# Optimization experiments

Hardware: AMD Instinct MI355X
Metric: run time of the kernel (lower is better)

Reference implementation:

```python
import jax, jax.numpy as jnp
import numpy as np

KMEANS_ITERS = 10  # fixed Lloyd iterations (original kmeans_pytorch iterates to tolerance)


def _assign(X, cent):
    # squared euclidean distances [N, K] (argmin identical to euclidean)
    d = (jnp.sum(X * X, axis=1, keepdims=True)
         - 2.0 * X @ cent.T
         + jnp.sum(cent * cent, axis=1)[None, :])
    return jnp.argmin(d, axis=1)


def _kmeans(X, K, iters, key):
    N, _ = X.shape
    init_idx = jax.random.choice(key, N, (K,), replace=False)
    cent0 = X[init_idx]

    def step(cent, _):
        idx = _assign(X, cent)
        sums = jax.ops.segment_sum(X, idx, num_segments=K)
        cnt = jax.ops.segment_sum(jnp.ones((N,), X.dtype), idx, num_segments=K)
        new = jnp.where(cnt[:, None] > 0,
                        sums / jnp.maximum(cnt, 1.0)[:, None],
                        cent)
        return new, None

    cent, _ = jax.lax.scan(step, cent0, None, length=iters)
    return _assign(X, cent)


def setup_inputs() -> dict:
    key = jax.random.key(0)
    B, L, D, H = 2, 4096, 256, 8
    k1, k2 = jax.random.split(key)
    qk = jax.random.normal(k1, (B, L, D), dtype=jnp.float32)
    # nn.init.orthogonal_ on (B, D, D): flatten to (B, D*D), make rows orthonormal.
    G = jax.random.normal(k2, (D * D, B), dtype=jnp.float32)
    Q, _ = jnp.linalg.qr(G)                # (D*D, B) orthonormal columns
    W_R = Q.T.reshape(B, D, D)             # rows orthonormal across batch
    return {"qk": qk, "W_R": W_R, "n_heads": H}


def reference(qk, W_R, n_heads):
    qk = jax.lax.stop_gradient(qk)          # qk.detach()
    B, L, D = qk.shape
    R = jnp.einsum('bld,bde->ble', qk, W_R).reshape(B * L, D)
    K = int(L ** 0.5)
    idx = _kmeans(R, K, KMEANS_ITERS, jax.random.key(42))
    cid = idx.reshape(B, L)
    # same-cluster mask [B, 1, L, L] broadcast to heads
    same = (cid[:, None, :, None] == cid[:, None, None, :])
    mask = jnp.broadcast_to(same, (B, n_heads, L, L)).astype(jnp.float32)
    return 10000.0 * mask - 10000.0
```

## Files before the change

kernel.cpp:

```cpp
#include <hip/hip_runtime.h>
#include <stdint.h>
#include <stddef.h>
#include <vector>
#include <algorithm>
#include <utility>

#define NPTS 8192
#define DIM  256
#define KC   64
#define LSEQ 4096
#define NB   2
#define KM_ITERS 10
#define NCHUNK 64
#define NBLK 128
#define NCENT 64
#define XPITCH 260
#define PPITCH 257

#define JAX_THREEFRY_PARTITIONABLE 1

__device__ float g_R[NPTS * DIM];
__device__ float g_xsq[NPTS];
__device__ float g_centT[DIM * KC];
__device__ float g_csq[KC];
__device__ int   g_idx[NPTS];

__device__ unsigned g_arrive[NBLK * 16];
__device__ unsigned g_release_arr[NBLK * 16];

__device__ __forceinline__ void grid_barrier(int c, unsigned target) {
  __syncthreads();
  const int t = threadIdx.x;
  if (t == 0) {
    __hip_atomic_store(&g_arrive[c * 16], target, __ATOMIC_RELEASE,
                       __HIP_MEMORY_SCOPE_AGENT);
  }
  if (c == 0) {
    if (t < NBLK) {
      while (__hip_atomic_load(&g_arrive[t * 16], __ATOMIC_RELAXED,
                               __HIP_MEMORY_SCOPE_AGENT) < target) {
        __builtin_amdgcn_s_sleep(1);
      }
    }
    __syncthreads();
    if (t < NBLK) {
      if (t == 0) {
        __builtin_amdgcn_fence(__ATOMIC_ACQUIRE, "agent");
        __builtin_amdgcn_fence(__ATOMIC_RELEASE, "agent");
      }
      __hip_atomic_store(&g_release_arr[t * 16], target, __ATOMIC_RELAXED,
                         __HIP_MEMORY_SCOPE_AGENT);
    }
  } else {
    if (t == 0) {
      while (__hip_atomic_load(&g_release_arr[c * 16], __ATOMIC_RELAXED,
                               __HIP_MEMORY_SCOPE_AGENT) < target) {
        __builtin_amdgcn_s_sleep(1);
      }
      __builtin_amdgcn_fence(__ATOMIC_ACQUIRE, "agent");
    }
  }
  __syncthreads();
}

static inline uint32_t rotl32(uint32_t x, int r) { return (x << r) | (x >> (32 - r)); }

static void threefry2x32(uint32_t k0, uint32_t k1, uint32_t x0, uint32_t x1,
                         uint32_t& o0, uint32_t& o1) {
  const uint32_t ks0 = k0, ks1 = k1, ks2 = k0 ^ k1 ^ 0x1BD11BDAu;
  const int r1[4] = {13, 15, 26, 6}, r2[4] = {17, 29, 16, 24};
  x0 += ks0; x1 += ks1;
  for (int i = 0; i < 4; ++i) { x0 += x1; x1 = rotl32(x1, r1[i]); x1 ^= x0; }
  x0 += ks1; x1 += ks2 + 1u;
  for (int i = 0; i < 4; ++i) { x0 += x1; x1 = rotl32(x1, r2[i]); x1 ^= x0; }
  x0 += ks2; x1 += ks0 + 2u;
  for (int i = 0; i < 4; ++i) { x0 += x1; x1 = rotl32(x1, r1[i]); x1 ^= x0; }
  x0 += ks0; x1 += ks1 + 3u;
  for (int i = 0; i < 4; ++i) { x0 += x1; x1 = rotl32(x1, r2[i]); x1 ^= x0; }
  x0 += ks1; x1 += ks2 + 4u;
  for (int i = 0; i < 4; ++i) { x0 += x1; x1 = rotl32(x1, r1[i]); x1 ^= x0; }
  x0 += ks2; x1 += ks0 + 5u;
  o0 = x0; o1 = x1;
}

struct InitIdx { int v[KC]; };

static InitIdx compute_init_indices() {
  uint32_t k0 = 0u, k1 = 42u;
  std::vector<int> val(NPTS);
  for (int i = 0; i < NPTS; ++i) val[i] = i;
  std::vector<std::pair<uint32_t, int>> kv(NPTS);
  for (int round = 0; round < 2; ++round) {
    uint32_t nk0, nk1, sk0, sk1;
#if JAX_THREEFRY_PARTITIONABLE
    threefry2x32(k0, k1, 0u, 0u, nk0, nk1);
    threefry2x32(k0, k1, 0u, 1u, sk0, sk1);
    k0 = nk0; k1 = nk1;
    for (int i = 0; i < NPTS; ++i) {
      uint32_t o0, o1;
      threefry2x32(sk0, sk1, 0u, (uint32_t)i, o0, o1);
      kv[i] = std::make_pair(o0 ^ o1, val[i]);
    }
#else
    uint32_t a0, a1, b0, b1;
    threefry2x32(k0, k1, 0u, 2u, a0, a1);
    threefry2x32(k0, k1, 1u, 3u, b0, b1);
    nk0 = a0; nk1 = b0; sk0 = a1; sk1 = b1;
    k0 = nk0; k1 = nk1;
    for (int i = 0; i < NPTS / 2; ++i) {
      uint32_t o0, o1;
      threefry2x32(sk0, sk1, (uint32_t)i, (uint32_t)(i + NPTS / 2), o0, o1);
      kv[i] = std::make_pair(o0, 0);
      kv[i + NPTS / 2] = std::make_pair(o1, 0);
    }
    for (int i = 0; i < NPTS; ++i) kv[i].second = val[i];
#endif
    std::stable_sort(kv.begin(), kv.end(),
                     [](const std::pair<uint32_t, int>& a,
                        const std::pair<uint32_t, int>& b) { return a.first < b.first; });
    for (int i = 0; i < NPTS; ++i) val[i] = kv[i].second;
  }
  InitIdx ii;
  for (int k = 0; k < KC; ++k) ii.v[k] = val[k];
  return ii;
}


__global__ void __launch_bounds__(256) k_R_xsq(const float* __restrict__ qk,
                                               const float* __restrict__ W) {
  __shared__ float q[8][DIM];
  const int blk = blockIdx.x;
  const int b = blk / (LSEQ / 8);
  const int r0 = (blk % (LSEQ / 8)) * 8;
  const int t = threadIdx.x;
  for (int r = 0; r < 8; ++r)
    q[r][t] = qk[((size_t)b * LSEQ + r0 + r) * DIM + t];
  __syncthreads();
  float acc[8] = {0.f, 0.f, 0.f, 0.f, 0.f, 0.f, 0.f, 0.f};
  const float* Wb = W + (size_t)b * DIM * DIM;
  for (int d = 0; d < DIM; ++d) {
    const float w = Wb[d * DIM + t];
#pragma unroll
    for (int r = 0; r < 8; ++r) acc[r] = fmaf(q[r][d], w, acc[r]);
  }
  for (int r = 0; r < 8; ++r)
    g_R[((size_t)b * LSEQ + r0 + r) * DIM + t] = acc[r];
  __syncthreads();
  for (int r = 0; r < 8; ++r) q[r][t] = acc[r];
  __syncthreads();
  const int w = t >> 6, lane = t & 63;
#pragma unroll
  for (int rr = 0; rr < 2; ++rr) {
    const int r = w * 2 + rr;
    const float4 x = *(const float4*)&q[r][lane * 4];
    float s = x.x * x.x + x.y * x.y + x.z * x.z + x.w * x.w;
    for (int o = 32; o > 0; o >>= 1) s += __shfl_xor(s, o);
    if (lane == 0) g_xsq[(size_t)b * LSEQ + r0 + r] = s;
  }
}

__global__ void __launch_bounds__(1024) k_kmeans(InitIdx ii) {
  __shared__ __align__(16) float CsBuf[NCHUNK * PPITCH];
  __shared__ __align__(16) float Xs[64 * XPITCH];
  __shared__ float red[256];
  __shared__ int cnt_s[NCHUNK];
  __shared__ unsigned base_s;
  const int t = threadIdx.x;
  const int c = blockIdx.x;
  const int p0 = c * 64;
  const int ptg = t >> 4;
  const int ctg = t & 15;
  const int ct = ctg * 4;

  if (t == 0)
    base_s = __hip_atomic_load(&g_arrive[c * 16], __ATOMIC_RELAXED,
                               __HIP_MEMORY_SCOPE_AGENT);

  for (int idx = t; idx < 64 * (DIM / 4); idx += 1024) {
    const int r = idx >> 6;
    const int dq = idx & 63;
    *(float4*)&Xs[r * XPITCH + dq * 4] =
        *(const float4*)(g_R + (size_t)(p0 + r) * DIM + dq * 4);
  }
  float xs_reg[2] = {0.f, 0.f};
  if (t < 512) {
    xs_reg[0] = g_xsq[p0 + ptg * 2 + 0];
    xs_reg[1] = g_xsq[p0 + ptg * 2 + 1];
  }
  __syncthreads();
  const unsigned base = base_s;
  unsigned bar = 0;

  float myc = 0.f;
  if (c < NCENT) {
    if (t < 256) {
      const float cv = g_R[(size_t)ii.v[c] * DIM + t];
      myc = cv;
      g_centT[t * KC + c] = cv;
      red[t] = cv * cv;
    }
    __syncthreads();
    for (int o = 128; o > 0; o >>= 1) {
      if (t < o) red[t] += red[t + o];
      __syncthreads();
    }
    if (t == 0) g_csq[c] = red[0];
  }
  grid_barrier(c, base + (++bar));

  for (int it = 0; it <= KM_ITERS; ++it) {
    const bool final_pass = (it == KM_ITERS);

    {
      float4* Cs4 = (float4*)CsBuf;
      const float4* T4 = (const float4*)g_centT;
      for (int i = t; i < (DIM * KC) / 4; i += 1024) Cs4[i] = T4[i];
    }
    __syncthreads();

    if (t < 512) {
      const float cs0 = g_csq[ct + 0];
      const float cs1 = g_csq[ct + 1];
      const float cs2 = g_csq[ct + 2];
      const float cs3 = g_csq[ct + 3];

      float acc[2][4];
#pragma unroll
      for (int r = 0; r < 2; ++r)
#pragma unroll
        for (int j = 0; j < 4; ++j) acc[r][j] = 0.f;

#pragma unroll 4
      for (int d = 0; d < DIM; d += 4) {
        const float4 cv0 = *(const float4*)&CsBuf[(d + 0) * 64 + ct];
        const float4 cv1 = *(const float4*)&CsBuf[(d + 1) * 64 + ct];
        const float4 cv2 = *(const float4*)&CsBuf[(d + 2) * 64 + ct];
        const float4 cv3 = *(const float4*)&CsBuf[(d + 3) * 64 + ct];
#pragma unroll
        for (int r = 0; r < 2; ++r) {
          const float4 x = *(const float4*)&Xs[(ptg * 2 + r) * XPITCH + d];
          acc[r][0] = fmaf(x.x, cv0.x, fmaf(x.y, cv1.x, fmaf(x.z, cv2.x, fmaf(x.w, cv3.x, acc[r][0]))));
          acc[r][1] = fmaf(x.x, cv0.y, fmaf(x.y, cv1.y, fmaf(x.z, cv2.y, fmaf(x.w, cv3.y, acc[r][1]))));
          acc[r][2] = fmaf(x.x, cv0.z, fmaf(x.y, cv1.z, fmaf(x.z, cv2.z, fmaf(x.w, cv3.z, acc[r][2]))));
          acc[r][3] = fmaf(x.x, cv0.w, fmaf(x.y, cv1.w, fmaf(x.z, cv2.w, fmaf(x.w, cv3.w, acc[r][3]))));
        }
      }

#pragma unroll
      for (int r = 0; r < 2; ++r) {
        const int pl = ptg * 2 + r;
        const float xs = xs_reg[r];
        float best = 3.4e38f;
        int bk = 0;
        {
          float v;
          v = (xs - 2.0f * acc[r][0]) + cs0; if (v < best) { best = v; bk = ct + 0; }
          v = (xs - 2.0f * acc[r][1]) + cs1; if (v < best) { best = v; bk = ct + 1; }
          v = (xs - 2.0f * acc[r][2]) + cs2; if (v < best) { best = v; bk = ct + 2; }
          v = (xs - 2.0f * acc[r][3]) + cs3; if (v < best) { best = v; bk = ct + 3; }
        }
#pragma unroll
        for (int o = 1; o < 16; o <<= 1) {
          const float ov = __shfl_xor(best, o);
          const int obk = __shfl_xor(bk, o);
          if (ov < best || (ov == best && obk < bk)) { best = ov; bk = obk; }
        }
        if (ctg == 0) g_idx[p0 + pl] = bk;
      }
    }
    if (final_pass) break;
    grid_barrier(c, base + (++bar));

    if (c < NCENT) {
      const int ch = t >> 4;
      const int dq = t & 15;
      float4 s[4];
#pragma unroll
      for (int q = 0; q < 4; ++q) s[q] = make_float4(0.f, 0.f, 0.f, 0.f);
      int cnt = 0;
      const int pb = ch * 128;
      for (int j4 = 0; j4 < 32; ++j4) {
        const int4 iv = *(const int4*)(g_idx + pb + j4 * 4);
        if (iv.x == c) {
          const float4* row = (const float4*)(g_R + (size_t)(pb + j4 * 4 + 0) * DIM) + dq * 4;
#pragma unroll
          for (int q = 0; q < 4; ++q) { const float4 x = row[q]; s[q].x += x.x; s[q].y += x.y; s[q].z += x.z; s[q].w += x.w; }
          ++cnt;
        }
        if (iv.y == c) {
          const float4* row = (const float4*)(g_R + (size_t)(pb + j4 * 4 + 1) * DIM) + dq * 4;
#pragma unroll
          for (int q = 0; q < 4; ++q) { const float4 x = row[q]; s[q].x += x.x; s[q].y += x.y; s[q].z += x.z; s[q].w += x.w; }
          ++cnt;
        }
        if (iv.z == c) {
          const float4* row = (const float4*)(g_R + (size_t)(pb + j4 * 4 + 2) * DIM) + dq * 4;
#pragma unroll
          for (int q = 0; q < 4; ++q) { const float4 x = row[q]; s[q].x += x.x; s[q].y += x.y; s[q].z += x.z; s[q].w += x.w; }
          ++cnt;
        }
        if (iv.w == c) {
          const float4* row = (const float4*)(g_R + (size_t)(pb + j4 * 4 + 3) * DIM) + dq * 4;
#pragma unroll
          for (int q = 0; q < 4; ++q) { const float4 x = row[q]; s[q].x += x.x; s[q].y += x.y; s[q].z += x.z; s[q].w += x.w; }
          ++cnt;
        }
      }
      float* part = CsBuf;
#pragma unroll
      for (int q = 0; q < 4; ++q)
        *(float4*)&part[ch * PPITCH + dq * 16 + q * 4] = s[q];
      if (dq == 0) cnt_s[ch] = cnt;
      __syncthreads();

      if (t < 256) {
        float ssum = 0.f;
#pragma unroll 4
        for (int c2 = 0; c2 < NCHUNK; ++c2) ssum += part[c2 * PPITCH + t];
        int ctot = 0;
#pragma unroll 4
        for (int c2 = 0; c2 < NCHUNK; ++c2) ctot += cnt_s[c2];
        const float nc = (ctot > 0) ? (ssum / (float)ctot) : myc;
        myc = nc;
        g_centT[t * KC + c] = nc;
        red[t] = nc * nc;
      }
      __syncthreads();
      for (int o = 128; o > 0; o >>= 1) {
        if (t < o) red[t] += red[t + o];
        __syncthreads();
      }
      if (t == 0) g_csq[c] = red[0];
    }
    grid_barrier(c, base + (++bar));
  }
}

__global__ void __launch_bounds__(256) k_mask(float* __restrict__ out, int H) {
  const int blk = blockIdx.x;
  const int tiles = LSEQ / 16;
  const int b = blk / (H * tiles);
  const int h = (blk / tiles) % H;
  const int tile = blk % tiles;
  const int t = threadIdx.x;
  __shared__ int cid[LSEQ];
  for (int j = t; j < LSEQ; j += 256) cid[j] = g_idx[b * LSEQ + j];
  __syncthreads();
  const size_t base = ((size_t)(b * H + h) * LSEQ + (size_t)tile * 16) * LSEQ;
  for (int r = 0; r < 16; ++r) {
    const int my = cid[tile * 16 + r];
    float4* orow = (float4*)(out + base + (size_t)r * LSEQ);
#pragma unroll
    for (int s = 0; s < 4; ++s) {
      const int c4 = s * 256 + t;
      const int j = c4 * 4;
      float4 v;
      v.x = (cid[j + 0] == my) ? 0.f : -10000.f;
      v.y = (cid[j + 1] == my) ? 0.f : -10000.f;
      v.z = (cid[j + 2] == my) ? 0.f : -10000.f;
      v.w = (cid[j + 3] == my) ? 0.f : -10000.f;
      orow[c4] = v;
    }
  }
}

extern "C" void kernel_launch(void* const* d_in, const int* in_sizes, int n_in,
                              void* d_out, int out_size, void* d_ws, size_t ws_size,
                              hipStream_t stream) {
  const float* qk = (const float*)d_in[0];
  const float* W = (const float*)d_in[1];
  const int H = out_size / (NB * LSEQ * LSEQ);

  const InitIdx ii = compute_init_indices();

  k_R_xsq<<<NB * (LSEQ / 8), 256, 0, stream>>>(qk, W);
  k_kmeans<<<NBLK, 1024, 0, stream>>>(ii);
  k_mask<<<NB * H * (LSEQ / 16), 256, 0, stream>>>((float*)d_out, H);
}
```

Measured before the change: 597.0 us.

## Replace centralized grid barrier with producer-consumer flags between assign and update phases

Drops the two-phase centralized grid barrier, where block 0 gathers arrivals and then releases everyone. In its place are per-block flags: assignment blocks publish an idx flag, and centroid-owning blocks publish a centroid flag. Consumers spin only on the flags they depend on. This cuts one round trip per barrier and lets non-centroid blocks go straight to waiting for centroids. It relies on correct release/acquire ordering, and the base value taken from g_flag_idx must stay consistent across launches.

```diff
diff --git a/kernel.cpp b/kernel.cpp
--- a/kernel.cpp
+++ b/kernel.cpp
@@ -25,43 +25,8 @@
 __device__ float g_csq[KC];
 __device__ int   g_idx[NPTS];
 
-__device__ unsigned g_arrive[NBLK * 16];
-__device__ unsigned g_release_arr[NBLK * 16];
-
-__device__ __forceinline__ void grid_barrier(int c, unsigned target) {
-  __syncthreads();
-  const int t = threadIdx.x;
-  if (t == 0) {
-    __hip_atomic_store(&g_arrive[c * 16], target, __ATOMIC_RELEASE,
-                       __HIP_MEMORY_SCOPE_AGENT);
-  }
-  if (c == 0) {
-    if (t < NBLK) {
-      while (__hip_atomic_load(&g_arrive[t * 16], __ATOMIC_RELAXED,
-                               __HIP_MEMORY_SCOPE_AGENT) < target) {
-        __builtin_amdgcn_s_sleep(1);
-      }
-    }
-    __syncthreads();
-    if (t < NBLK) {
-      if (t == 0) {
-        __builtin_amdgcn_fence(__ATOMIC_ACQUIRE, "agent");
-        __builtin_amdgcn_fence(__ATOMIC_RELEASE, "agent");
-      }
-      __hip_atomic_store(&g_release_arr[t * 16], target, __ATOMIC_RELAXED,
-                         __HIP_MEMORY_SCOPE_AGENT);
-    }
-  } else {
-    if (t == 0) {
-      while (__hip_atomic_load(&g_release_arr[c * 16], __ATOMIC_RELAXED,
-                               __HIP_MEMORY_SCOPE_AGENT) < target) {
-        __builtin_amdgcn_s_sleep(1);
-      }
-      __builtin_amdgcn_fence(__ATOMIC_ACQUIRE, "agent");
-    }
-  }
-  __syncthreads();
-}
+__device__ unsigned g_flag_idx[NBLK * 16];
+__device__ unsigned g_flag_cent[NCENT * 16];
 
 static inline uint32_t rotl32(uint32_t x, int r) { return (x << r) | (x >> (32 - r)); }
 
@@ -173,7 +138,7 @@
   const int ct = ctg * 4;
 
   if (t == 0)
-    base_s = __hip_atomic_load(&g_arrive[c * 16], __ATOMIC_RELAXED,
+    base_s = __hip_atomic_load(&g_flag_idx[c * 16], __ATOMIC_RELAXED,
                                __HIP_MEMORY_SCOPE_AGENT);
 
   for (int idx = t; idx < 64 * (DIM / 4); idx += 1024) {
@@ -189,7 +154,6 @@
   }
   __syncthreads();
   const unsigned base = base_s;
-  unsigned bar = 0;
 
   float myc = 0.f;
   if (c < NCENT) {
@@ -204,12 +168,27 @@
       if (t < o) red[t] += red[t + o];
       __syncthreads();
     }
-    if (t == 0) g_csq[c] = red[0];
-  }
-  grid_barrier(c, base + (++bar));
+    if (t == 0) {
+      g_csq[c] = red[0];
+    }
+    __syncthreads();
+    if (t == 0)
+      __hip_atomic_store(&g_flag_cent[c * 16], base + 1u, __ATOMIC_RELEASE,
+                         __HIP_MEMORY_SCOPE_AGENT);
+  }
 
   for (int it = 0; it <= KM_ITERS; ++it) {
-    const bool final_pass = (it == KM_ITERS);
+    const unsigned tgt = base + (unsigned)(it + 1);
+
+    if (t < NCENT) {
+      while (__hip_atomic_load(&g_flag_cent[t * 16], __ATOMIC_RELAXED,
+                               __HIP_MEMORY_SCOPE_AGENT) < tgt) {
+        __builtin_amdgcn_s_sleep(1);
+      }
+    }
+    __syncthreads();
+    if (t == 0) __builtin_amdgcn_fence(__ATOMIC_ACQUIRE, "agent");
+    __syncthreads();
 
     {
       float4* Cs4 = (float4*)CsBuf;
@@ -268,10 +247,23 @@
         if (ctg == 0) g_idx[p0 + pl] = bk;
       }
     }
-    if (final_pass) break;
-    grid_barrier(c, base + (++bar));
+    __syncthreads();
+    if (t == 0)
+      __hip_atomic_store(&g_flag_idx[c * 16], tgt, __ATOMIC_RELEASE,
+                         __HIP_MEMORY_SCOPE_AGENT);
+    if (it == KM_ITERS) break;
 
     if (c < NCENT) {
+      if (t < NBLK) {
+        while (__hip_atomic_load(&g_flag_idx[t * 16], __ATOMIC_RELAXED,
+                                 __HIP_MEMORY_SCOPE_AGENT) < tgt) {
+          __builtin_amdgcn_s_sleep(1);
+        }
+      }
+      __syncthreads();
+      if (t == 0) __builtin_amdgcn_fence(__ATOMIC_ACQUIRE, "agent");
+      __syncthreads();
+
       const int ch = t >> 4;
       const int dq = t & 15;
       float4 s[4];
@@ -331,8 +323,11 @@
         __syncthreads();
       }
       if (t == 0) g_csq[c] = red[0];
-    }
-    grid_barrier(c, base + (++bar));
+      __syncthreads();
+      if (t == 0)
+        __hip_atomic_store(&g_flag_cent[c * 16], tgt + 1u, __ATOMIC_RELEASE,
+                           __HIP_MEMORY_SCOPE_AGENT);
+    }
   }
 }
 
```

New measurement: 595.7 us. No clear change (-0.2%).
